# Kernel optimization log

Measured on AMD Instinct MI355X. Metric: run time of the kernel, lower is better.

The kernel has to match this reference:

```python
import jax, jax.numpy as jnp
import numpy as np

D = 256          # embed_dim
NH = 4           # num_heads
NE = 16          # num_hyperedges
TC = 512         # text_channels
WIN = 64         # window size
EPS = 1e-5


def setup_inputs() -> dict:
    key = jax.random.key(0)
    ks = jax.random.split(key, 20)
    s = 0.02
    return {
        "feature_map": jax.random.normal(ks[0], (8, 256, 64, 64), jnp.float32),
        "text_features": jax.random.normal(ks[1], (8, 64, TC), jnp.float32),
        # qkv_gen: Conv2d(256->256,1x1), GELU, Conv2d(256->768,3x3,pad1), GroupNorm(4,768)
        "conv1_w": jax.random.normal(ks[2], (D, 256, 1, 1), jnp.float32) * s,
        "conv1_b": jnp.zeros((D,), jnp.float32),
        "conv2_w": jax.random.normal(ks[3], (3 * D, D, 3, 3), jnp.float32) * s,
        "conv2_b": jnp.zeros((3 * D,), jnp.float32),
        "gn_w": jnp.ones((3 * D,), jnp.float32),
        "gn_b": jnp.zeros((3 * D,), jnp.float32),
        # shared nn.MultiheadAttention params
        "in_proj_w": jax.random.normal(ks[4], (3 * D, D), jnp.float32) * s,
        "in_proj_b": jnp.zeros((3 * D,), jnp.float32),
        "out_proj_w": jax.random.normal(ks[5], (D, D), jnp.float32) * s,
        "out_proj_b": jnp.zeros((D,), jnp.float32),
        # text_adapter Linear(512->256)
        "txt_w": jax.random.normal(ks[6], (D, TC), jnp.float32) * s,
        "txt_b": jnp.zeros((D,), jnp.float32),
        # edge_predictor: Linear(512->256), GELU, Linear(256->16)
        "ep1_w": jax.random.normal(ks[7], (D, 2 * D), jnp.float32) * s,
        "ep1_b": jnp.zeros((D,), jnp.float32),
        "ep2_w": jax.random.normal(ks[8], (NE, D), jnp.float32) * s,
        "ep2_b": jnp.zeros((NE,), jnp.float32),
    }


def _gelu(x):
    return jax.nn.gelu(x, approximate=False)  # torch default is exact erf GELU


def _conv(x, w, b, pad):
    y = jax.lax.conv_general_dilated(x, w, (1, 1), [(pad, pad), (pad, pad)],
                                     dimension_numbers=("NCHW", "OIHW", "NCHW"))
    return y + b[None, :, None, None]


def _group_norm(x, w, b, groups=4):
    B, C, H, W = x.shape
    xg = x.reshape(B, groups, C // groups, H, W)
    mu = xg.mean(axis=(2, 3, 4), keepdims=True)
    var = xg.var(axis=(2, 3, 4), keepdims=True)
    xg = (xg - mu) * jax.lax.rsqrt(var + EPS)
    return xg.reshape(B, C, H, W) * w[None, :, None, None] + b[None, :, None, None]


def _mha(q, k, v, in_w, in_b, out_w, out_b):
    # torch nn.MultiheadAttention (batch_first), same-dim q/k/v
    Wq, Wk, Wv = in_w[:D], in_w[D:2 * D], in_w[2 * D:]
    bq, bk, bv = in_b[:D], in_b[D:2 * D], in_b[2 * D:]
    dh = D // NH

    def split(x, W, bias):
        y = x @ W.T + bias                      # [B,L,D]
        Bv, L, _ = y.shape
        return y.reshape(Bv, L, NH, dh).transpose(0, 2, 1, 3)  # [B,H,L,dh]

    qh, kh, vh = split(q, Wq, bq), split(k, Wk, bk), split(v, Wv, bv)
    scores = jnp.einsum("bhqd,bhkd->bhqk", qh, kh) / jnp.sqrt(jnp.float32(dh))
    attn = jax.nn.softmax(scores, axis=-1)
    o = jnp.einsum("bhqk,bhkd->bhqd", attn, vh)
    Bv, _, Lq, _ = o.shape
    o = o.transpose(0, 2, 1, 3).reshape(Bv, Lq, D)
    return o @ out_w.T + out_b


def reference(feature_map, text_features, conv1_w, conv1_b, conv2_w, conv2_b,
              gn_w, gn_b, in_proj_w, in_proj_b, out_proj_w, out_proj_b,
              txt_w, txt_b, ep1_w, ep1_b, ep2_w, ep2_b):
    B, C, H, W = feature_map.shape
    N = H * W
    # qkv_gen
    x = _gelu(_conv(feature_map, conv1_w, conv1_b, 0))
    qkv = _group_norm(_conv(x, conv2_w, conv2_b, 1), gn_w, gn_b)
    q, k, v = jnp.split(qkv, 3, axis=1)                    # each [B,D,H,W]
    to_seq = lambda t: t.reshape(B, D, N).transpose(0, 2, 1)  # [B,N,D]
    q_seq, k_seq, v_seq = to_seq(q), to_seq(k), to_seq(v)

    # text_adapter: Linear then AdaptiveAvgPool1d(4) over sequence (L=64 -> 4 bins of 16)
    t = text_features @ txt_w.T + txt_b                    # [B,L,D]
    L = t.shape[1]
    text_feat = t.reshape(B, 4, L // 4, D).mean(axis=2)    # [B,4,D]

    # hierarchical attention
    nw = N // WIN
    q_win = q_seq.reshape(B * nw, WIN, D)
    k_win = k_seq.reshape(B * nw, WIN, D)
    v_win = v_seq.reshape(B * nw, WIN, D)
    local = _mha(q_win, k_win, v_win, in_proj_w, in_proj_b, out_proj_w, out_proj_b)
    local = local.reshape(B, nw, WIN, D)
    global_q = local.mean(axis=2)                          # [B,nw,D]
    glob = _mha(global_q, text_feat, text_feat, in_proj_w, in_proj_b, out_proj_w, out_proj_b)
    glob = jnp.broadcast_to(glob[:, :, None, :], (B, nw, WIN, D))

    combined = jnp.concatenate([local.reshape(B, N, D), glob.reshape(B, N, D)], axis=-1)
    h = _gelu(combined @ ep1_w.T + ep1_b)
    return jax.nn.sigmoid(h @ ep2_w.T + ep2_b)             # [B,N,16]
```

## Files before the change

### kernel.cpp

```cpp
#include <hip/hip_runtime.h>

#define DEV __device__ __forceinline__

typedef __attribute__((ext_vector_type(8))) short bfx8;
typedef __attribute__((ext_vector_type(4))) float fx4;

typedef __attribute__((address_space(3))) unsigned int as3_u32;
typedef const __attribute__((address_space(1))) unsigned int as1_u32c;

DEV void gl_lds16(const void* g, const void* l) {
  __builtin_amdgcn_global_load_lds((as1_u32c*)(unsigned long long)g,
                                   (as3_u32*)(unsigned long long)l, 16, 0, 0);
}

DEV short f2bf(float f) {
  unsigned u = __float_as_uint(f);
  u += 0x7fffu + ((u >> 16) & 1u);
  return (short)(u >> 16);
}
DEV float bf2f(short s) {
  return __uint_as_float(((unsigned)(unsigned short)s) << 16);
}
DEV float gelu_f(float x) { return 0.5f * x * (1.0f + erff(x * 0.70710678118654752f)); }

#define MFMA16(acc, a, b) (acc) = __builtin_amdgcn_mfma_f32_16x16x32_bf16((a), (b), (acc), 0, 0, 0)

struct CvtSeg { const float* src; short* dst; int n; };
struct CvtArgs { CvtSeg s[7]; };

__global__ __launch_bounds__(256) void cvt_multi(CvtArgs a) {
  CvtSeg s = a.s[blockIdx.y];
  int i = ((int)blockIdx.x * 256 + (int)threadIdx.x) * 8;
  if (i >= s.n) return;
  bfx8 o;
  #pragma unroll
  for (int j = 0; j < 8; ++j) o[j] = f2bf(s.src[i + j]);
  *(bfx8*)(s.dst + i) = o;
}

__global__ __launch_bounds__(256) void cvt_conv2w(const float* src, short* dst) {
  int oc = (int)blockIdx.x * 256 + (int)threadIdx.x;
  const float* s = src + (long)oc * 9;
  float t[9];
  #pragma unroll
  for (int j = 0; j < 9; ++j) t[j] = s[j];
  #pragma unroll
  for (int tap = 0; tap < 9; ++tap)
    dst[(long)tap * (768 * 256) + oc] = f2bf(t[tap]);
}

__global__ __launch_bounds__(64) void ebc2(const float* e1w, const float* e1b, const float* ob, float* ebc) {
  int n = blockIdx.x, lane = threadIdx.x;
  float s = 0.0f;
  #pragma unroll
  for (int i = 0; i < 4; ++i) {
    int c = lane + 64 * i;
    s += ob[c] * e1w[(long)n * 512 + c];
  }
  #pragma unroll
  for (int off = 1; off < 64; off <<= 1) s += __shfl_xor(s, off);
  if (lane == 0) ebc[n] = e1b[n] + s;
}

__global__ __launch_bounds__(256) void wcombk(const float* ow, const short* Wep1, short* Wcomb) {
  __shared__ short Bt[64 * 264];
  const int t = threadIdx.x;
  const int lane = t & 63, w = t >> 6;
  const int lg = lane >> 4, li = lane & 15;
  const int m0 = blockIdx.y * 64, n0 = blockIdx.x * 64;
  for (int idx = t; idx < 64 * 256; idx += 256) {
    int c = idx >> 6, d = idx & 63;
    Bt[d * 264 + c] = f2bf(ow[(long)c * 256 + n0 + d]);
  }
  __syncthreads();
  fx4 acc[4] = {};
  const short* aR = Wep1 + (long)(m0 + w * 16 + li) * 512 + lg * 8;
  for (int kc = 0; kc < 256; kc += 32) {
    bfx8 a = *(const bfx8*)(aR + kc);
    #pragma unroll
    for (int ni = 0; ni < 4; ++ni) {
      bfx8 bv = *(const bfx8*)(&Bt[(ni * 16 + li) * 264 + kc + lg * 8]);
      MFMA16(acc[ni], a, bv);
    }
  }
  #pragma unroll
  for (int ni = 0; ni < 4; ++ni)
    #pragma unroll
    for (int r = 0; r < 4; ++r)
      Wcomb[(long)(m0 + w * 16 + 4 * lg + r) * 256 + n0 + ni * 16 + li] = f2bf(acc[ni][r]);
}

DEV int axc(int p, int c) { return p * 260 + (c ^ (((p >> 2) & 7) << 2)); }

__global__ __launch_bounds__(256) void tc1(const float* fm, const short* W1bf,
                                           const float* b1, short* xP) {
  __shared__ float Af[64 * 260];
  const int lane = threadIdx.x & 63, wv = threadIdx.x >> 6;
  const int lg = lane >> 4, li = lane & 15;
  const int y = blockIdx.x & 63, b = blockIdx.x >> 6;
  const int t = threadIdx.x;
  short* dstP = xP + ((long)b * 66 * 66 + (long)(y + 1) * 66 + 1) * 256;
  const bfx8 z8 = {0, 0, 0, 0, 0, 0, 0, 0};

  if (t < 64) {
    if (t < 32) *(bfx8*)(dstP - 256 + t * 8) = z8;
    else        *(bfx8*)(dstP + 64 * 256 + (t - 32) * 8) = z8;
  }
  if (y == 0) {
    short* top = xP + (long)b * 66 * 66 * 256;
    for (int i = t; i < 2112; i += 256) *(bfx8*)(top + i * 8) = z8;
  }
  if (y == 63) {
    short* bot = xP + ((long)b * 66 * 66 + 65 * 66) * 256;
    for (int i = t; i < 2112; i += 256) *(bfx8*)(bot + i * 8) = z8;
  }

  const float* src = fm + (long)b * 256 * 4096 + y * 64;
  #pragma unroll
  for (int i = 0; i < 16; ++i) {
    int chunk = i * 256 + t;
    int c = chunk >> 4;
    int q = chunk & 15;
    fx4 v = *(const fx4*)(src + (long)c * 4096 + q * 4);
    #pragma unroll
    for (int j = 0; j < 4; ++j) Af[axc(q * 4 + j, c)] = v[j];
  }
  __syncthreads();

  fx4 acc[4][4] = {};
  const short* Bb = W1bf + (long)(wv * 64 + li) * 256 + lg * 8;
  for (int c0 = 0; c0 < 256; c0 += 32) {
    bfx8 af[4], bfr[4];
    #pragma unroll
    for (int mi = 0; mi < 4; ++mi) {
      int p = mi * 16 + li;
      fx4 lo = *(const fx4*)(&Af[axc(p, c0 + lg * 8)]);
      fx4 hi = *(const fx4*)(&Af[axc(p, c0 + lg * 8 + 4)]);
      bfx8 tt;
      tt[0] = f2bf(lo[0]); tt[1] = f2bf(lo[1]); tt[2] = f2bf(lo[2]); tt[3] = f2bf(lo[3]);
      tt[4] = f2bf(hi[0]); tt[5] = f2bf(hi[1]); tt[6] = f2bf(hi[2]); tt[7] = f2bf(hi[3]);
      af[mi] = tt;
    }
    #pragma unroll
    for (int ni = 0; ni < 4; ++ni) bfr[ni] = *(const bfx8*)(Bb + ni * 16 * 256 + c0);
    #pragma unroll
    for (int mi = 0; mi < 4; ++mi)
      #pragma unroll
      for (int ni = 0; ni < 4; ++ni) MFMA16(acc[mi][ni], af[mi], bfr[ni]);
  }

  #pragma unroll
  for (int mi = 0; mi < 4; ++mi)
    #pragma unroll
    for (int ni = 0; ni < 4; ++ni) {
      int col = wv * 64 + ni * 16 + li;
      float bias = b1[col];
      #pragma unroll
      for (int r = 0; r < 4; ++r) {
        int x = mi * 16 + 4 * lg + r;
        dstP[(long)x * 256 + col] = f2bf(gelu_f(acc[mi][ni][r] + bias));
      }
    }
}

struct GemmP {
  const short* A; const short* B; void* O;
  const float* biasN; const float* biasM; const float* rowbias;
  long lda, ldb, ldo, sA, sB, sO;
  int M, N, K, outF32, act, padHW;
  int aShift;
  long sBN, sBM;
};

DEV void gemm_body(const GemmP& g, int bx, int by, int bz) {
  __shared__ short As[128 * 32];
  __shared__ short Bs[128 * 32];
  const int lane = threadIdx.x & 63, wv = threadIdx.x >> 6;
  const int wm = wv >> 1, wn = wv & 1;
  const int lg = lane >> 4, li = lane & 15;
  const int m0 = by * 128, n0 = bx * 128, z = bz;
  const short* A = g.A + (long)z * g.sA + (long)(n0 >> 8) * g.aShift;
  const short* B = g.B + (long)z * g.sB;
  const int srow = wv * 16 + (lane >> 2);
  const int scol = (lane & 3) * 8;
  const short* pA0 = A + (long)(m0 + srow) * g.lda + scol;
  const short* pA1 = A + (long)(m0 + 64 + srow) * g.lda + scol;
  const short* pB0 = B + (long)(n0 + srow) * g.ldb + scol;
  const short* pB1 = B + (long)(n0 + 64 + srow) * g.ldb + scol;
  short* ldsA = As + wv * 512;
  short* ldsB = Bs + wv * 512;
  const short* aRd = As + (wm * 64 + li) * 32 + lg * 8;
  const short* bRd = Bs + (wn * 64 + li) * 32 + lg * 8;

  fx4 acc[4][4] = {};
  for (int kc = 0; kc < g.K; kc += 32) {
    gl_lds16(pA0 + kc, ldsA);
    gl_lds16(pA1 + kc, ldsA + 2048);
    gl_lds16(pB0 + kc, ldsB);
    gl_lds16(pB1 + kc, ldsB + 2048);
    __syncthreads();
    bfx8 af[4], bf[4];
    #pragma unroll
    for (int mi = 0; mi < 4; ++mi) af[mi] = *(const bfx8*)(aRd + mi * 16 * 32);
    #pragma unroll
    for (int ni = 0; ni < 4; ++ni) bf[ni] = *(const bfx8*)(bRd + ni * 16 * 32);
    #pragma unroll
    for (int mi = 0; mi < 4; ++mi)
      #pragma unroll
      for (int ni = 0; ni < 4; ++ni)
        MFMA16(acc[mi][ni], af[mi], bf[ni]);
    __syncthreads();
  }

  #pragma unroll
  for (int mi = 0; mi < 4; ++mi)
    #pragma unroll
    for (int ni = 0; ni < 4; ++ni) {
      int col = n0 + wn * 64 + ni * 16 + li;
      int rowb = m0 + wm * 64 + mi * 16 + 4 * lg;
      float bn = g.biasN ? g.biasN[(long)z * g.sBN + col] : 0.0f;
      #pragma unroll
      for (int r = 0; r < 4; ++r) {
        int row = rowb + r;
        float v = acc[mi][ni][r] + bn;
        if (g.biasM) v += g.biasM[(long)z * g.sBM + row];
        if (g.act == 1) v = gelu_f(v);
        long oidx = (long)z * g.sO + (long)row * g.ldo + col;
        if (g.outF32) ((float*)g.O)[oidx] = v;
        else ((short*)g.O)[oidx] = f2bf(v);
      }
    }
}

__global__ __launch_bounds__(256) void projk(GemmP gq, GemmP gv) {
  int bid = (int)blockIdx.x;
  int id = (bid & 7) * 192 + (bid >> 3);
  if (id < 1024) {
    int z = id >> 7, r = id & 127;
    gemm_body(gq, r & 3, r >> 2, z);
  } else {
    int j = id - 1024;
    int z = j >> 6, r = j & 63;
    gemm_body(gv, r & 31, r >> 5, z);
  }
}

__global__ __launch_bounds__(256) void conv2g(const short* xP, const short* W2t,
                                              const float* b2, short* qkv, float* stats) {
  __shared__ short As[2 * 128 * 32];
  __shared__ short Bs[2 * 128 * 32];
  __shared__ float red[4][4];
  const int lane = threadIdx.x & 63, wv = threadIdx.x >> 6;
  const int wm = wv >> 1, wn = wv & 1;
  const int lg = lane >> 4, li = lane & 15;
  const int w = ((int)blockIdx.x & 7) * 192 + ((int)blockIdx.x >> 3);
  const int n0 = (w % 6) * 128;
  const int by = w / 6;
  const int b = by >> 5, ypair = by & 31;
  const short* xPb = xP + (long)b * 66 * 66 * 256;

  const int srow = wv * 16 + (lane >> 2);
  const int scol = (lane & 3) * 8;
  long baseA[2], baseB[2];
  #pragma unroll
  for (int j = 0; j < 2; ++j) {
    int r = j * 64 + srow;
    int yy = 2 * ypair + (r >> 6);
    int x = r & 63;
    baseA[j] = ((long)yy * 66 + x) * 256 + scol;
    baseB[j] = (long)(n0 + r) * 256 + scol;
  }
  short* ldsA = As + wv * 512;
  short* ldsB = Bs + wv * 512;
  const short* aRd = As + (wm * 64 + li) * 32 + lg * 8;
  const short* bRd = Bs + (wn * 64 + li) * 32 + lg * 8;

  fx4 acc[4][4] = {};
  for (int ks = 0; ks < 36; ++ks) {
    int tap = ks >> 2;
    int c0 = (ks & 3) * 64;
    int dy = tap / 3, dx = tap - dy * 3;
    long aoff = (long)(dy * 66 + dx) * 256 + c0;
    long boff = (long)tap * (768 * 256) + c0;
    gl_lds16(xPb + baseA[0] + aoff, ldsA);
    gl_lds16(xPb + baseA[1] + aoff, ldsA + 2048);
    gl_lds16(xPb + baseA[0] + aoff + 32, ldsA + 4096);
    gl_lds16(xPb + baseA[1] + aoff + 32, ldsA + 6144);
    gl_lds16(W2t + baseB[0] + boff, ldsB);
    gl_lds16(W2t + baseB[1] + boff, ldsB + 2048);
    gl_lds16(W2t + baseB[0] + boff + 32, ldsB + 4096);
    gl_lds16(W2t + baseB[1] + boff + 32, ldsB + 6144);
    __syncthreads();
    #pragma unroll
    for (int kk = 0; kk < 2; ++kk) {
      bfx8 af[4], bf[4];
      #pragma unroll
      for (int mi = 0; mi < 4; ++mi) af[mi] = *(const bfx8*)(aRd + kk * 4096 + mi * 16 * 32);
      #pragma unroll
      for (int ni = 0; ni < 4; ++ni) bf[ni] = *(const bfx8*)(bRd + kk * 4096 + ni * 16 * 32);
      #pragma unroll
      for (int mi = 0; mi < 4; ++mi)
        #pragma unroll
        for (int ni = 0; ni < 4; ++ni)
          MFMA16(acc[mi][ni], af[mi], bf[ni]);
    }
    __syncthreads();
  }

  const int g0 = n0 / 192;
  const int bnd = (g0 + 1) * 192;
  float sA = 0.0f, s2A = 0.0f, sB = 0.0f, s2B = 0.0f;
  const long prow0 = (long)b * 4096 + (long)ypair * 128 + wm * 64 + 4 * lg;
  #pragma unroll
  for (int ni = 0; ni < 4; ++ni) {
    int col = n0 + wn * 64 + ni * 16 + li;
    float bias = b2[col];
    bool inA = (col < bnd);
    #pragma unroll
    for (int mi = 0; mi < 4; ++mi) {
      long rb = prow0 + mi * 16;
      #pragma unroll
      for (int r = 0; r < 4; ++r) {
        float v = acc[mi][ni][r] + bias;
        if (inA) { sA += v; s2A += v * v; } else { sB += v; s2B += v * v; }
        qkv[(rb + r) * 768 + col] = f2bf(v);
      }
    }
  }
  #pragma unroll
  for (int off = 1; off < 64; off <<= 1) {
    sA += __shfl_xor(sA, off);  s2A += __shfl_xor(s2A, off);
    sB += __shfl_xor(sB, off);  s2B += __shfl_xor(s2B, off);
  }
  if (lane == 0) { red[wv][0] = sA; red[wv][1] = s2A; red[wv][2] = sB; red[wv][3] = s2B; }
  __syncthreads();
  if (threadIdx.x == 0) {
    float a1 = red[0][0] + red[1][0] + red[2][0] + red[3][0];
    float a2 = red[0][1] + red[1][1] + red[2][1] + red[3][1];
    atomicAdd(&stats[(b * 4 + g0) * 2], a1);
    atomicAdd(&stats[(b * 4 + g0) * 2 + 1], a2);
    if (bnd < n0 + 128) {
      float b1s = red[0][2] + red[1][2] + red[2][2] + red[3][2];
      float b2s = red[0][3] + red[1][3] + red[2][3] + red[3][3];
      atomicAdd(&stats[(b * 4 + g0 + 1) * 2], b1s);
      atomicAdd(&stats[(b * 4 + g0 + 1) * 2 + 1], b2s);
    }
  }
}

__global__ __launch_bounds__(256) void gn_fold(const float* stats, const float* gnw, const float* gnb,
                                               const float* inw, const float* inb,
                                               short* Wf, float* bfold) {
  const int lane = threadIdx.x & 63, wv = threadIdx.x >> 6;
  const int row = blockIdx.x * 4 + wv;
  const int b = row / 768, j = row - b * 768;
  const int cb = (j >> 8) << 8;
  const float nrm = 1.0f / (192.0f * 4096.0f);
  float part = 0.0f;
  #pragma unroll
  for (int i = 0; i < 4; ++i) {
    int c = lane + 64 * i;
    int cg = cb + c;
    int grp = cg / 192;
    float s1 = stats[(b * 4 + grp) * 2];
    float s2 = stats[(b * 4 + grp) * 2 + 1];
    float mu = s1 * nrm;
    float var = s2 * nrm - mu * mu;
    float rs = rsqrtf(var + 1e-5f);
    float s = rs * gnw[cg];
    float t = gnb[cg] - mu * s;
    float wv_ = inw[(long)j * 256 + c];
    Wf[(long)row * 256 + c] = f2bf(wv_ * s);
    part += t * wv_;
  }
  #pragma unroll
  for (int off = 1; off < 64; off <<= 1) part += __shfl_xor(part, off);
  if (lane == 0) bfold[row] = inb[j] + part;
}

__global__ __launch_bounds__(256) void globk_txt(const short* Tbf, const short* Wtxt,
                                                 const short* Wqkv, const float* tb,
                                                 const float* inb, float* khv, float* vhv) {
  __shared__ float tmean_s[4][512];
  __shared__ float tfb_s[4][256];
  const int t = threadIdx.x;
  const int b = blockIdx.x;
  {
    int key = t >> 6, d0 = (t & 63) * 8;
    float s[8] = {};
    const short* src = Tbf + ((long)(b * 64 + key * 16)) * 512 + d0;
    for (int i = 0; i < 16; ++i) {
      bfx8 v = *(const bfx8*)(src + i * 512);
      #pragma unroll
      for (int j = 0; j < 8; ++j) s[j] += bf2f(v[j]);
    }
    #pragma unroll
    for (int j = 0; j < 8; ++j) tmean_s[key][d0 + j] = s[j] * (1.0f / 16.0f);
  }
  __syncthreads();
  {
    int n = t;
    float a0 = 0, a1 = 0, a2 = 0, a3 = 0;
    const short* wr = Wtxt + (long)n * 512;
    for (int d = 0; d < 512; d += 8) {
      bfx8 w = *(const bfx8*)(wr + d);
      #pragma unroll
      for (int j = 0; j < 8; ++j) {
        float wf = bf2f(w[j]);
        a0 += tmean_s[0][d + j] * wf;
        a1 += tmean_s[1][d + j] * wf;
        a2 += tmean_s[2][d + j] * wf;
        a3 += tmean_s[3][d + j] * wf;
      }
    }
    float bias = tb[n];
    tfb_s[0][n] = a0 + bias; tfb_s[1][n] = a1 + bias;
    tfb_s[2][n] = a2 + bias; tfb_s[3][n] = a3 + bias;
  }
  __syncthreads();
  {
    int n = t;
    const short* wk = Wqkv + (long)(256 + n) * 256;
    const short* wvp = Wqkv + (long)(512 + n) * 256;
    float k0=0,k1=0,k2=0,k3=0,v0=0,v1=0,v2=0,v3=0;
    for (int d = 0; d < 256; d += 8) {
      bfx8 wkv = *(const bfx8*)(wk + d);
      bfx8 wvv = *(const bfx8*)(wvp + d);
      #pragma unroll
      for (int j = 0; j < 8; ++j) {
        float f0 = tfb_s[0][d+j], f1 = tfb_s[1][d+j], f2 = tfb_s[2][d+j], f3 = tfb_s[3][d+j];
        float kw = bf2f(wkv[j]), vw = bf2f(wvv[j]);
        k0 += f0*kw; k1 += f1*kw; k2 += f2*kw; k3 += f3*kw;
        v0 += f0*vw; v1 += f1*vw; v2 += f2*vw; v3 += f3*vw;
      }
    }
    float bk = inb[256+n], bv = inb[512+n];
    khv[(b*4+0)*256+n]=k0+bk; khv[(b*4+1)*256+n]=k1+bk;
    khv[(b*4+2)*256+n]=k2+bk; khv[(b*4+3)*256+n]=k3+bk;
    vhv[(b*4+0)*256+n]=v0+bv; vhv[(b*4+1)*256+n]=v1+bv;
    vhv[(b*4+2)*256+n]=v2+bv; vhv[(b*4+3)*256+n]=v3+bv;
  }
}

__global__ __launch_bounds__(256) void attn_local(const short* qk, const short* vhT,
                                                  short* oat, short* oatm) {
  __shared__ short Pl[4 * 64 * 72];
  const int lane = threadIdx.x & 63, h = threadIdx.x >> 6;
  const int lg = lane >> 4, li = lane & 15;
  const int bw = blockIdx.x;
  const int b = bw >> 6, wY = bw & 63;
  const long p0 = (long)bw * 64;

  bfx8 qf[4][2], kf[4][2];
  #pragma unroll
  for (int mi = 0; mi < 4; ++mi)
    #pragma unroll
    for (int ks = 0; ks < 2; ++ks) {
      qf[mi][ks] = *(const bfx8*)(qk + (p0 + 16 * mi + li) * 512 + h * 64 + 32 * ks + 8 * lg);
      kf[mi][ks] = *(const bfx8*)(qk + (p0 + 16 * mi + li) * 512 + 256 + h * 64 + 32 * ks + 8 * lg);
    }
  fx4 s[4][4] = {};
  #pragma unroll
  for (int mi = 0; mi < 4; ++mi)
    #pragma unroll
    for (int ni = 0; ni < 4; ++ni) {
      MFMA16(s[mi][ni], qf[mi][0], kf[ni][0]);
      MFMA16(s[mi][ni], qf[mi][1], kf[ni][1]);
    }
  #pragma unroll
  for (int mi = 0; mi < 4; ++mi)
    #pragma unroll
    for (int ni = 0; ni < 4; ++ni) s[mi][ni] *= 0.125f;

  #pragma unroll
  for (int mi = 0; mi < 4; ++mi)
    #pragma unroll
    for (int r = 0; r < 4; ++r) {
      float mx = fmaxf(fmaxf(s[mi][0][r], s[mi][1][r]), fmaxf(s[mi][2][r], s[mi][3][r]));
      for (int off = 1; off < 16; off <<= 1) mx = fmaxf(mx, __shfl_xor(mx, off));
      float e[4];
      float sum = 0.0f;
      #pragma unroll
      for (int ni = 0; ni < 4; ++ni) { e[ni] = expf(s[mi][ni][r] - mx); sum += e[ni]; }
      for (int off = 1; off < 16; off <<= 1) sum += __shfl_xor(sum, off);
      float inv = 1.0f / sum;
      int row = h * 64 + 16 * mi + 4 * lg + r;
      #pragma unroll
      for (int ni = 0; ni < 4; ++ni) Pl[row * 72 + 16 * ni + li] = f2bf(e[ni] * inv);
    }
  __syncthreads();

  fx4 o[4][4] = {};
  #pragma unroll
  for (int ks = 0; ks < 2; ++ks) {
    bfx8 pf[4], vf[4];
    #pragma unroll
    for (int mi = 0; mi < 4; ++mi)
      pf[mi] = *(const bfx8*)(&Pl[(h * 64 + 16 * mi + li) * 72 + 32 * ks + 8 * lg]);
    #pragma unroll
    for (int ni = 0; ni < 4; ++ni)
      vf[ni] = *(const bfx8*)(vhT + ((long)(b * 256 + h * 64 + 16 * ni + li)) * 4096 + wY * 64 + 32 * ks + 8 * lg);
    #pragma unroll
    for (int mi = 0; mi < 4; ++mi)
      #pragma unroll
      for (int ni = 0; ni < 4; ++ni) MFMA16(o[mi][ni], pf[mi], vf[ni]);
  }
  #pragma unroll
  for (int mi = 0; mi < 4; ++mi)
    #pragma unroll
    for (int ni = 0; ni < 4; ++ni)
      #pragma unroll
      for (int r = 0; r < 4; ++r)
        oat[(p0 + 16 * mi + 4 * lg + r) * 256 + h * 64 + 16 * ni + li] = f2bf(o[mi][ni][r]);

  #pragma unroll
  for (int ni = 0; ni < 4; ++ni) {
    float s2 = 0.0f;
    #pragma unroll
    for (int mi = 0; mi < 4; ++mi)
      #pragma unroll
      for (int r = 0; r < 4; ++r) s2 += o[mi][ni][r];
    s2 += __shfl_xor(s2, 16);
    s2 += __shfl_xor(s2, 32);
    if (lg == 0)
      oatm[(long)bw * 256 + h * 64 + 16 * ni + li] = f2bf(s2 * (1.0f / 64.0f));
  }
}

#define GP 272

DEV void mm_stage(const short* srcA, const short* Bw, long ldb, const float* biasN,
                  short* dstL, float* dstG, int wv, int lg, int li) {
  fx4 acc[4][4] = {};
  const short* aRd = srcA + li * GP + lg * 8;
  const short* bR = Bw + (long)(wv * 64 + li) * ldb + lg * 8;
  for (int kc = 0; kc < 256; kc += 32) {
    bfx8 af[4], bf[4];
    #pragma unroll
    for (int mi = 0; mi < 4; ++mi) af[mi] = *(const bfx8*)(aRd + mi * 16 * GP + kc);
    #pragma unroll
    for (int ni = 0; ni < 4; ++ni) bf[ni] = *(const bfx8*)(bR + (long)ni * 16 * ldb + kc);
    #pragma unroll
    for (int mi = 0; mi < 4; ++mi)
      #pragma unroll
      for (int ni = 0; ni < 4; ++ni) MFMA16(acc[mi][ni], af[mi], bf[ni]);
  }
  #pragma unroll
  for (int mi = 0; mi < 4; ++mi)
    #pragma unroll
    for (int ni = 0; ni < 4; ++ni) {
      int col = wv * 64 + ni * 16 + li;
      float bn = biasN[col];
      #pragma unroll
      for (int r = 0; r < 4; ++r) {
        int row = mi * 16 + 4 * lg + r;
        float v = acc[mi][ni][r] + bn;
        if (dstL) dstL[row * GP + col] = f2bf(v);
        else dstG[(long)row * 256 + col] = v;
      }
    }
}

__global__ __launch_bounds__(256) void globk2(
    const short* oatm, const float* khv, const float* vhv,
    const short* Wo, const short* Wqkv, const short* Wep1,
    const float* ob, const float* inb, const float* ebc,
    float* gcon) {
  __shared__ short bufA[64 * GP];
  __shared__ short bufB[64 * GP];
  __shared__ float kh_s[4][256];
  __shared__ float vh_s[4][256];
  __shared__ float scb[16], pb[16];
  const int t = threadIdx.x;
  const int lane = t & 63, wv = t >> 6;
  const int lg = lane >> 4, li = lane & 15;
  const int b = blockIdx.x;

  {
    #pragma unroll
    for (int i = 0; i < 8; ++i) {
      int chunk = i * 256 + t;
      int row = chunk >> 5, colc = (chunk & 31) * 8;
      *(bfx8*)(bufA + row * GP + colc) =
          *(const bfx8*)(oatm + ((long)(b * 64 + row)) * 256 + colc);
    }
    #pragma unroll
    for (int key = 0; key < 4; ++key) {
      kh_s[key][t] = khv[(long)(b * 4 + key) * 256 + t];
      vh_s[key][t] = vhv[(long)(b * 4 + key) * 256 + t];
    }
  }
  __syncthreads();
  mm_stage(bufA, Wo, 256, ob, bufB, nullptr, wv, lg, li);
  __syncthreads();
  mm_stage(bufB, Wqkv, 256, inb, bufA, nullptr, wv, lg, li);
  __syncthreads();
  {
    int p = t >> 2, h = t & 3;
    const short* qr = bufA + p * GP + h * 64;
    float sc[4];
    #pragma unroll
    for (int key = 0; key < 4; ++key) {
      float s = 0.0f;
      for (int d = 0; d < 64; d += 8) {
        bfx8 q8 = *(const bfx8*)(qr + d);
        #pragma unroll
        for (int j = 0; j < 8; ++j) s += bf2f(q8[j]) * kh_s[key][h * 64 + d + j];
      }
      sc[key] = s * 0.125f;
    }
    float mx = fmaxf(fmaxf(sc[0], sc[1]), fmaxf(sc[2], sc[3]));
    float e0 = expf(sc[0]-mx), e1 = expf(sc[1]-mx), e2 = expf(sc[2]-mx), e3 = expf(sc[3]-mx);
    float inv = 1.0f / (e0 + e1 + e2 + e3);
    e0 *= inv; e1 *= inv; e2 *= inv; e3 *= inv;
    short* orow = bufB + p * GP + h * 64;
    for (int d = 0; d < 64; ++d) {
      float o = e0*vh_s[0][h*64+d] + e1*vh_s[1][h*64+d] + e2*vh_s[2][h*64+d] + e3*vh_s[3][h*64+d];
      orow[d] = f2bf(o);
    }
  }
  __syncthreads();
  mm_stage(bufB, Wo, 256, ob, bufA, nullptr, wv, lg, li);
  __syncthreads();
  mm_stage(bufA, Wep1 + 256, 512, ebc, nullptr, gcon + (long)b * 64 * 256, wv, lg, li);
}

__global__ __launch_bounds__(256) void ep12(const short* oat, const short* Wcomb,
                                            const short* Wep2, const float* gcon,
                                            const float* e2b, float* out) {
  __shared__ short As[128 * 32];
  __shared__ short Bs[128 * 32];
  __shared__ short hl[128 * 140];
  const int lane = threadIdx.x & 63, wv = threadIdx.x >> 6;
  const int wm = wv >> 1, wn = wv & 1;
  const int lg = lane >> 4, li = lane & 15;
  const int m0 = (int)blockIdx.x * 128;
  const int srow = wv * 16 + (lane >> 2);
  const int scol = (lane & 3) * 8;
  const short* pA0 = oat + (long)(m0 + srow) * 256 + scol;
  const short* pA1 = oat + (long)(m0 + 64 + srow) * 256 + scol;
  short* ldsA = As + wv * 512;
  short* ldsB = Bs + wv * 512;
  const short* aRd = As + (wm * 64 + li) * 32 + lg * 8;
  const short* bRd = Bs + (wn * 64 + li) * 32 + lg * 8;

  fx4 eacc[2] = {};
  for (int half = 0; half < 2; ++half) {
    const short* B = Wcomb + (long)(half * 128) * 256;
    const short* pB0 = B + (long)srow * 256 + scol;
    const short* pB1 = B + (long)(64 + srow) * 256 + scol;
    fx4 acc[4][4] = {};
    for (int kc = 0; kc < 256; kc += 32) {
      gl_lds16(pA0 + kc, ldsA);
      gl_lds16(pA1 + kc, ldsA + 2048);
      gl_lds16(pB0 + kc, ldsB);
      gl_lds16(pB1 + kc, ldsB + 2048);
      __syncthreads();
      bfx8 af[4], bf[4];
      #pragma unroll
      for (int mi = 0; mi < 4; ++mi) af[mi] = *(const bfx8*)(aRd + mi * 16 * 32);
      #pragma unroll
      for (int ni = 0; ni < 4; ++ni) bf[ni] = *(const bfx8*)(bRd + ni * 16 * 32);
      #pragma unroll
      for (int mi = 0; mi < 4; ++mi)
        #pragma unroll
        for (int ni = 0; ni < 4; ++ni)
          MFMA16(acc[mi][ni], af[mi], bf[ni]);
      __syncthreads();
    }
    #pragma unroll
    for (int mi = 0; mi < 4; ++mi)
      #pragma unroll
      for (int ni = 0; ni < 4; ++ni) {
        int coll = wn * 64 + ni * 16 + li;
        int colg = half * 128 + coll;
        #pragma unroll
        for (int r = 0; r < 4; ++r) {
          int rowl = wm * 64 + mi * 16 + 4 * lg + r;
          float v = acc[mi][ni][r] + gcon[(long)((m0 + rowl) >> 6) * 256 + colg];
          hl[rowl * 140 + coll] = f2bf(gelu_f(v));
        }
      }
    __syncthreads();
    #pragma unroll
    for (int kc = 0; kc < 128; kc += 32) {
      bfx8 bf2v = *(const bfx8*)(Wep2 + (long)li * 256 + half * 128 + kc + lg * 8);
      #pragma unroll
      for (int mi = 0; mi < 2; ++mi) {
        bfx8 af = *(const bfx8*)(hl + (wv * 32 + mi * 16 + li) * 140 + kc + lg * 8);
        MFMA16(eacc[mi], af, bf2v);
      }
    }
    __syncthreads();
  }
  #pragma unroll
  for (int mi = 0; mi < 2; ++mi)
    #pragma unroll
    for (int r = 0; r < 4; ++r) {
      int row = m0 + wv * 32 + mi * 16 + 4 * lg + r;
      out[(long)row * 16 + li] = 1.0f / (1.0f + expf(-(eacc[mi][r] + e2b[li])));
    }
}

extern "C" void kernel_launch(void* const* d_in, const int* in_sizes, int n_in,
                              void* d_out, int out_size, void* d_ws, size_t ws_size,
                              hipStream_t stream) {
  (void)in_sizes; (void)n_in; (void)out_size; (void)ws_size;
  const float* fm  = (const float*)d_in[0];
  const float* txt = (const float*)d_in[1];
  const float* w1  = (const float*)d_in[2];
  const float* b1  = (const float*)d_in[3];
  const float* w2  = (const float*)d_in[4];
  const float* b2  = (const float*)d_in[5];
  const float* gnw = (const float*)d_in[6];
  const float* gnb = (const float*)d_in[7];
  const float* inw = (const float*)d_in[8];
  const float* inb = (const float*)d_in[9];
  const float* ow  = (const float*)d_in[10];
  const float* ob  = (const float*)d_in[11];
  const float* tw  = (const float*)d_in[12];
  const float* tb  = (const float*)d_in[13];
  const float* e1w = (const float*)d_in[14];
  const float* e1b = (const float*)d_in[15];
  const float* e2w = (const float*)d_in[16];
  const float* e2b = (const float*)d_in[17];
  float* out = (float*)d_out;

  char* base = (char*)d_ws;
  size_t off = 0;
  auto alloc = [&](size_t bytes) -> char* {
    char* r = base + off;
    off = (off + bytes + 255) & ~(size_t)255;
    return r;
  };
  short* W1bf = (short*)alloc(256 * 256 * 2);
  short* W2t  = (short*)alloc((size_t)9 * 768 * 256 * 2);
  short* Wqkv = (short*)alloc(768 * 256 * 2);
  short* Wo   = (short*)alloc(256 * 256 * 2);
  short* Wcomb= (short*)alloc(256 * 256 * 2);
  float* ebc  = (float*)alloc(256 * 4);
  short* Wtxt = (short*)alloc(256 * 512 * 2);
  short* Wep1 = (short*)alloc(256 * 512 * 2);
  short* Wep2 = (short*)alloc(16 * 256 * 2);
  short* Tbf  = (short*)alloc((size_t)8 * 64 * 512 * 2);
  short* xP   = (short*)alloc((size_t)8 * 66 * 66 * 256 * 2);
  short* qkv  = (short*)alloc((size_t)8 * 4096 * 768 * 2);
  float* stats= (float*)alloc(64 * 4);
  short* Wf   = (short*)alloc((size_t)8 * 768 * 256 * 2);
  float* bfold= (float*)alloc((size_t)8 * 768 * 4);
  short* qk   = (short*)alloc((size_t)32768 * 512 * 2);
  short* vhT  = (short*)alloc((size_t)8 * 4096 * 256 * 2);
  short* oat  = (short*)alloc((size_t)8 * 4096 * 256 * 2);
  short* oatm = (short*)alloc(512 * 256 * 2);
  float* khv  = (float*)alloc(8 * 4 * 256 * 4);
  float* vhv  = (float*)alloc(8 * 4 * 256 * 4);
  float* gcon = (float*)alloc(512 * 256 * 4);

  hipMemsetAsync(stats, 0, 64 * 4, stream);

  CvtArgs ca;
  ca.s[0] = {w1,  W1bf, 256 * 256};
  ca.s[1] = {inw, Wqkv, 768 * 256};
  ca.s[2] = {ow,  Wo,   256 * 256};
  ca.s[3] = {tw,  Wtxt, 256 * 512};
  ca.s[4] = {e1w, Wep1, 256 * 512};
  ca.s[5] = {e2w, Wep2, 16 * 256};
  ca.s[6] = {txt, Tbf,  8 * 64 * 512};
  cvt_multi<<<dim3(128, 7), 256, 0, stream>>>(ca);
  cvt_conv2w<<<768, 256, 0, stream>>>(w2, W2t);
  ebc2<<<256, 64, 0, stream>>>(e1w, e1b, ob, ebc);
  globk_txt<<<8, 256, 0, stream>>>(Tbf, Wtxt, Wqkv, tb, inb, khv, vhv);
  wcombk<<<dim3(4, 4), 256, 0, stream>>>(ow, Wep1, Wcomb);

  tc1<<<512, 256, 0, stream>>>(fm, W1bf, b1, xP);

  conv2g<<<1536, 256, 0, stream>>>(xP, W2t, b2, qkv, stats);

  gn_fold<<<1536, 256, 0, stream>>>(stats, gnw, gnb, inw, inb, Wf, bfold);

  {
    GemmP gq{};
    gq.A = qkv; gq.lda = 768; gq.sA = 4096L * 768;
    gq.B = Wf; gq.ldb = 256; gq.sB = 768L * 256;
    gq.O = qk; gq.ldo = 512; gq.sO = 4096L * 512;
    gq.biasN = bfold; gq.sBN = 768;
    gq.aShift = 256;
    gq.M = 4096; gq.N = 512; gq.K = 256;
    GemmP gv{};
    gv.A = Wf + 512 * 256; gv.lda = 256; gv.sA = 768L * 256;
    gv.B = qkv + 512; gv.ldb = 768; gv.sB = 4096L * 768;
    gv.O = vhT; gv.ldo = 4096; gv.sO = 256L * 4096;
    gv.biasM = bfold + 512; gv.sBM = 768;
    gv.M = 256; gv.N = 4096; gv.K = 256;
    projk<<<1536, 256, 0, stream>>>(gq, gv);
  }

  attn_local<<<512, 256, 0, stream>>>(qk, vhT, oat, oatm);

  globk2<<<8, 256, 0, stream>>>(oatm, khv, vhv, Wo, Wqkv, Wep1, ob, inb, ebc, gcon);

  ep12<<<256, 256, 0, stream>>>(oat, Wcomb, Wep2, gcon, e2b, out);
}
```

Before: 328.5 us.

## Merge prep kernels, fuse global attention into local attention, deepen GEMM K-step

Folds the five weight-conversion and text-projection kernels into one multi-role prep kernel, with the text path computed from fp32 inputs directly so the text-to-bf16 conversion is gone. The global-attention kernel now runs as the tail of the local-attention kernel: the last block per batch, picked by an atomic counter, does the global stage. GEMM and ep12 main loops load 64-wide K slices per barrier instead of 32, and the conv2 loop uses incremental offsets instead of per-iteration division. The aim is fewer launches, fewer barriers and fewer serialized tiny kernels, at the cost of larger LDS use and a counter-based handoff that relies on threadfences.

```diff
diff --git a/kernel.cpp b/kernel.cpp
--- a/kernel.cpp
+++ b/kernel.cpp
@@ -25,69 +25,142 @@
 
 #define MFMA16(acc, a, b) (acc) = __builtin_amdgcn_mfma_f32_16x16x32_bf16((a), (b), (acc), 0, 0, 0)
 
-struct CvtSeg { const float* src; short* dst; int n; };
-struct CvtArgs { CvtSeg s[7]; };
-
-__global__ __launch_bounds__(256) void cvt_multi(CvtArgs a) {
-  CvtSeg s = a.s[blockIdx.y];
-  int i = ((int)blockIdx.x * 256 + (int)threadIdx.x) * 8;
-  if (i >= s.n) return;
-  bfx8 o;
-  #pragma unroll
-  for (int j = 0; j < 8; ++j) o[j] = f2bf(s.src[i + j]);
-  *(bfx8*)(s.dst + i) = o;
-}
-
-__global__ __launch_bounds__(256) void cvt_conv2w(const float* src, short* dst) {
-  int oc = (int)blockIdx.x * 256 + (int)threadIdx.x;
-  const float* s = src + (long)oc * 9;
-  float t[9];
-  #pragma unroll
-  for (int j = 0; j < 9; ++j) t[j] = s[j];
-  #pragma unroll
-  for (int tap = 0; tap < 9; ++tap)
-    dst[(long)tap * (768 * 256) + oc] = f2bf(t[tap]);
-}
-
-__global__ __launch_bounds__(64) void ebc2(const float* e1w, const float* e1b, const float* ob, float* ebc) {
-  int n = blockIdx.x, lane = threadIdx.x;
-  float s = 0.0f;
-  #pragma unroll
-  for (int i = 0; i < 4; ++i) {
-    int c = lane + 64 * i;
-    s += ob[c] * e1w[(long)n * 512 + c];
-  }
-  #pragma unroll
-  for (int off = 1; off < 64; off <<= 1) s += __shfl_xor(s, off);
-  if (lane == 0) ebc[n] = e1b[n] + s;
-}
-
-__global__ __launch_bounds__(256) void wcombk(const float* ow, const short* Wep1, short* Wcomb) {
-  __shared__ short Bt[64 * 264];
+struct PrepArgs {
+  const float *w1, *inw, *ow, *tw, *e1w, *e2w, *txt, *w2, *e1b, *ob, *tb, *inb;
+  short *W1bf, *Wqkv, *Wo, *Wtxt, *Wep1, *Wep2, *W2t, *Wcomb;
+  float *ebc, *khv, *vhv;
+};
+
+__global__ __launch_bounds__(256) void prep(PrepArgs a) {
+  __shared__ char shmem[34816];
+  const int bid = (int)blockIdx.x;
   const int t = threadIdx.x;
-  const int lane = t & 63, w = t >> 6;
-  const int lg = lane >> 4, li = lane & 15;
-  const int m0 = blockIdx.y * 64, n0 = blockIdx.x * 64;
-  for (int idx = t; idx < 64 * 256; idx += 256) {
-    int c = idx >> 6, d = idx & 63;
-    Bt[d * 264 + c] = f2bf(ow[(long)c * 256 + n0 + d]);
-  }
-  __syncthreads();
-  fx4 acc[4] = {};
-  const short* aR = Wep1 + (long)(m0 + w * 16 + li) * 512 + lg * 8;
-  for (int kc = 0; kc < 256; kc += 32) {
-    bfx8 a = *(const bfx8*)(aR + kc);
-    #pragma unroll
-    for (int ni = 0; ni < 4; ++ni) {
-      bfx8 bv = *(const bfx8*)(&Bt[(ni * 16 + li) * 264 + kc + lg * 8]);
-      MFMA16(acc[ni], a, bv);
-    }
-  }
-  #pragma unroll
-  for (int ni = 0; ni < 4; ++ni)
-    #pragma unroll
-    for (int r = 0; r < 4; ++r)
-      Wcomb[(long)(m0 + w * 16 + 4 * lg + r) * 256 + n0 + ni * 16 + li] = f2bf(acc[ni][r]);
+  if (bid < 290) {
+    const float* src; short* dst; int st;
+    if (bid < 32)       { src = a.w1;  dst = a.W1bf; st = 0; }
+    else if (bid < 128) { src = a.inw; dst = a.Wqkv; st = 32; }
+    else if (bid < 160) { src = a.ow;  dst = a.Wo;   st = 128; }
+    else if (bid < 224) { src = a.tw;  dst = a.Wtxt; st = 160; }
+    else if (bid < 288) { src = a.e1w; dst = a.Wep1; st = 224; }
+    else                { src = a.e2w; dst = a.Wep2; st = 288; }
+    long i = ((long)(bid - st) * 256 + t) * 8;
+    bfx8 o;
+    #pragma unroll
+    for (int j = 0; j < 8; ++j) o[j] = f2bf(src[i + j]);
+    *(bfx8*)(dst + i) = o;
+  } else if (bid < 1058) {
+    int oc = (bid - 290) * 256 + t;
+    const float* s = a.w2 + (long)oc * 9;
+    float v[9];
+    #pragma unroll
+    for (int j = 0; j < 9; ++j) v[j] = s[j];
+    #pragma unroll
+    for (int tap = 0; tap < 9; ++tap)
+      a.W2t[(long)tap * (768 * 256) + oc] = f2bf(v[tap]);
+  } else if (bid < 1122) {
+    int n = (bid - 1058) * 4 + (t >> 6);
+    int lane = t & 63;
+    float s = 0.0f;
+    #pragma unroll
+    for (int i = 0; i < 4; ++i) {
+      int c = lane + 64 * i;
+      s += a.ob[c] * a.e1w[(long)n * 512 + c];
+    }
+    #pragma unroll
+    for (int off = 1; off < 64; off <<= 1) s += __shfl_xor(s, off);
+    if (lane == 0) a.ebc[n] = a.e1b[n] + s;
+  } else if (bid < 1130) {
+    float* tmean = (float*)shmem;
+    float* tfb = (float*)(shmem + 8192);
+    const int b = bid - 1122;
+    {
+      int key = t >> 6, d0 = (t & 63) * 8;
+      float s[8] = {};
+      const float* src = a.txt + ((long)(b * 64 + key * 16)) * 512 + d0;
+      for (int i = 0; i < 16; ++i) {
+        fx4 v0 = *(const fx4*)(src + (long)i * 512);
+        fx4 v1 = *(const fx4*)(src + (long)i * 512 + 4);
+        #pragma unroll
+        for (int j = 0; j < 4; ++j) { s[j] += v0[j]; s[4 + j] += v1[j]; }
+      }
+      #pragma unroll
+      for (int j = 0; j < 8; ++j) tmean[key * 512 + d0 + j] = s[j] * (1.0f / 16.0f);
+    }
+    __syncthreads();
+    {
+      int n = t;
+      float a0 = 0, a1 = 0, a2 = 0, a3 = 0;
+      const float* wr = a.tw + (long)n * 512;
+      for (int d = 0; d < 512; d += 4) {
+        fx4 w = *(const fx4*)(wr + d);
+        #pragma unroll
+        for (int j = 0; j < 4; ++j) {
+          float wf = w[j];
+          a0 += tmean[0 * 512 + d + j] * wf;
+          a1 += tmean[1 * 512 + d + j] * wf;
+          a2 += tmean[2 * 512 + d + j] * wf;
+          a3 += tmean[3 * 512 + d + j] * wf;
+        }
+      }
+      float bias = a.tb[n];
+      tfb[0 * 256 + n] = a0 + bias; tfb[1 * 256 + n] = a1 + bias;
+      tfb[2 * 256 + n] = a2 + bias; tfb[3 * 256 + n] = a3 + bias;
+    }
+    __syncthreads();
+    {
+      int n = t;
+      const float* wk = a.inw + (long)(256 + n) * 256;
+      const float* wvp = a.inw + (long)(512 + n) * 256;
+      float k0=0,k1=0,k2=0,k3=0,v0=0,v1=0,v2=0,v3=0;
+      for (int d = 0; d < 256; d += 4) {
+        fx4 wkv = *(const fx4*)(wk + d);
+        fx4 wvv = *(const fx4*)(wvp + d);
+        #pragma unroll
+        for (int j = 0; j < 4; ++j) {
+          float f0 = tfb[0*256+d+j], f1 = tfb[1*256+d+j], f2 = tfb[2*256+d+j], f3 = tfb[3*256+d+j];
+          float kw = wkv[j], vw = wvv[j];
+          k0 += f0*kw; k1 += f1*kw; k2 += f2*kw; k3 += f3*kw;
+          v0 += f0*vw; v1 += f1*vw; v2 += f2*vw; v3 += f3*vw;
+        }
+      }
+      float bk = a.inb[256+n], bv = a.inb[512+n];
+      a.khv[(b*4+0)*256+n]=k0+bk; a.khv[(b*4+1)*256+n]=k1+bk;
+      a.khv[(b*4+2)*256+n]=k2+bk; a.khv[(b*4+3)*256+n]=k3+bk;
+      a.vhv[(b*4+0)*256+n]=v0+bv; a.vhv[(b*4+1)*256+n]=v1+bv;
+      a.vhv[(b*4+2)*256+n]=v2+bv; a.vhv[(b*4+3)*256+n]=v3+bv;
+    }
+  } else {
+    short* Bt = (short*)shmem;
+    const int idx = bid - 1130;
+    const int bx = idx & 3, by = idx >> 2;
+    const int lane = t & 63, w = t >> 6;
+    const int lg = lane >> 4, li = lane & 15;
+    const int m0 = by * 64, n0 = bx * 64;
+    for (int id2 = t; id2 < 64 * 256; id2 += 256) {
+      int c = id2 >> 6, d = id2 & 63;
+      Bt[d * 264 + c] = f2bf(a.ow[(long)c * 256 + n0 + d]);
+    }
+    __syncthreads();
+    fx4 acc[4] = {};
+    const float* aR = a.e1w + (long)(m0 + w * 16 + li) * 512 + lg * 8;
+    for (int kc = 0; kc < 256; kc += 32) {
+      fx4 lo = *(const fx4*)(aR + kc);
+      fx4 hi = *(const fx4*)(aR + kc + 4);
+      bfx8 av;
+      av[0] = f2bf(lo[0]); av[1] = f2bf(lo[1]); av[2] = f2bf(lo[2]); av[3] = f2bf(lo[3]);
+      av[4] = f2bf(hi[0]); av[5] = f2bf(hi[1]); av[6] = f2bf(hi[2]); av[7] = f2bf(hi[3]);
+      #pragma unroll
+      for (int ni = 0; ni < 4; ++ni) {
+        bfx8 bv = *(const bfx8*)(&Bt[(ni * 16 + li) * 264 + kc + lg * 8]);
+        MFMA16(acc[ni], av, bv);
+      }
+    }
+    #pragma unroll
+    for (int ni = 0; ni < 4; ++ni)
+      #pragma unroll
+      for (int r = 0; r < 4; ++r)
+        a.Wcomb[(long)(m0 + w * 16 + 4 * lg + r) * 256 + n0 + ni * 16 + li] = f2bf(acc[ni][r]);
+  }
 }
 
 DEV int axc(int p, int c) { return p * 260 + (c ^ (((p >> 2) & 7) << 2)); }
@@ -165,16 +238,16 @@
 
 struct GemmP {
   const short* A; const short* B; void* O;
-  const float* biasN; const float* biasM; const float* rowbias;
+  const float* biasN; const float* biasM;
   long lda, ldb, ldo, sA, sB, sO;
-  int M, N, K, outF32, act, padHW;
+  int M, N, K, outF32, act;
   int aShift;
   long sBN, sBM;
 };
 
-DEV void gemm_body(const GemmP& g, int bx, int by, int bz) {
-  __shared__ short As[128 * 32];
-  __shared__ short Bs[128 * 32];
+DEV void gemm_body64(const GemmP& g, int bx, int by, int bz) {
+  __shared__ short As[2 * 128 * 32];
+  __shared__ short Bs[2 * 128 * 32];
   const int lane = threadIdx.x & 63, wv = threadIdx.x >> 6;
   const int wm = wv >> 1, wn = wv & 1;
   const int lg = lane >> 4, li = lane & 15;
@@ -193,22 +266,29 @@
   const short* bRd = Bs + (wn * 64 + li) * 32 + lg * 8;
 
   fx4 acc[4][4] = {};
-  for (int kc = 0; kc < g.K; kc += 32) {
+  for (int kc = 0; kc < g.K; kc += 64) {
     gl_lds16(pA0 + kc, ldsA);
     gl_lds16(pA1 + kc, ldsA + 2048);
+    gl_lds16(pA0 + kc + 32, ldsA + 4096);
+    gl_lds16(pA1 + kc + 32, ldsA + 6144);
     gl_lds16(pB0 + kc, ldsB);
     gl_lds16(pB1 + kc, ldsB + 2048);
+    gl_lds16(pB0 + kc + 32, ldsB + 4096);
+    gl_lds16(pB1 + kc + 32, ldsB + 6144);
     __syncthreads();
-    bfx8 af[4], bf[4];
-    #pragma unroll
-    for (int mi = 0; mi < 4; ++mi) af[mi] = *(const bfx8*)(aRd + mi * 16 * 32);
-    #pragma unroll
-    for (int ni = 0; ni < 4; ++ni) bf[ni] = *(const bfx8*)(bRd + ni * 16 * 32);
-    #pragma unroll
-    for (int mi = 0; mi < 4; ++mi)
-      #pragma unroll
-      for (int ni = 0; ni < 4; ++ni)
-        MFMA16(acc[mi][ni], af[mi], bf[ni]);
+    #pragma unroll
+    for (int kk = 0; kk < 2; ++kk) {
+      bfx8 af[4], bf[4];
+      #pragma unroll
+      for (int mi = 0; mi < 4; ++mi) af[mi] = *(const bfx8*)(aRd + kk * 4096 + mi * 16 * 32);
+      #pragma unroll
+      for (int ni = 0; ni < 4; ++ni) bf[ni] = *(const bfx8*)(bRd + kk * 4096 + ni * 16 * 32);
+      #pragma unroll
+      for (int mi = 0; mi < 4; ++mi)
+        #pragma unroll
+        for (int ni = 0; ni < 4; ++ni)
+          MFMA16(acc[mi][ni], af[mi], bf[ni]);
+    }
     __syncthreads();
   }
 
@@ -237,11 +317,11 @@
   int id = (bid & 7) * 192 + (bid >> 3);
   if (id < 1024) {
     int z = id >> 7, r = id & 127;
-    gemm_body(gq, r & 3, r >> 2, z);
+    gemm_body64(gq, r & 3, r >> 2, z);
   } else {
     int j = id - 1024;
     int z = j >> 6, r = j & 63;
-    gemm_body(gv, r & 31, r >> 5, z);
+    gemm_body64(gv, r & 31, r >> 5, z);
   }
 }
 
@@ -276,12 +356,9 @@
   const short* bRd = Bs + (wn * 64 + li) * 32 + lg * 8;
 
   fx4 acc[4][4] = {};
+  long aoff = 0, boff = 0;
+  int txc = 0;
   for (int ks = 0; ks < 36; ++ks) {
-    int tap = ks >> 2;
-    int c0 = (ks & 3) * 64;
-    int dy = tap / 3, dx = tap - dy * 3;
-    long aoff = (long)(dy * 66 + dx) * 256 + c0;
-    long boff = (long)tap * (768 * 256) + c0;
     gl_lds16(xPb + baseA[0] + aoff, ldsA);
     gl_lds16(xPb + baseA[1] + aoff, ldsA + 2048);
     gl_lds16(xPb + baseA[0] + aoff + 32, ldsA + 4096);
@@ -305,6 +382,12 @@
           MFMA16(acc[mi][ni], af[mi], bf[ni]);
     }
     __syncthreads();
+    aoff += 64; boff += 64;
+    if ((ks & 3) == 3) {
+      boff += 196608 - 256;
+      if (txc == 2) { aoff += 16128; txc = 0; }
+      else ++txc;
+    }
   }
 
   const int g0 = n0 / 192;
@@ -378,155 +461,6 @@
   if (lane == 0) bfold[row] = inb[j] + part;
 }
 
-__global__ __launch_bounds__(256) void globk_txt(const short* Tbf, const short* Wtxt,
-                                                 const short* Wqkv, const float* tb,
-                                                 const float* inb, float* khv, float* vhv) {
-  __shared__ float tmean_s[4][512];
-  __shared__ float tfb_s[4][256];
-  const int t = threadIdx.x;
-  const int b = blockIdx.x;
-  {
-    int key = t >> 6, d0 = (t & 63) * 8;
-    float s[8] = {};
-    const short* src = Tbf + ((long)(b * 64 + key * 16)) * 512 + d0;
-    for (int i = 0; i < 16; ++i) {
-      bfx8 v = *(const bfx8*)(src + i * 512);
-      #pragma unroll
-      for (int j = 0; j < 8; ++j) s[j] += bf2f(v[j]);
-    }
-    #pragma unroll
-    for (int j = 0; j < 8; ++j) tmean_s[key][d0 + j] = s[j] * (1.0f / 16.0f);
-  }
-  __syncthreads();
-  {
-    int n = t;
-    float a0 = 0, a1 = 0, a2 = 0, a3 = 0;
-    const short* wr = Wtxt + (long)n * 512;
-    for (int d = 0; d < 512; d += 8) {
-      bfx8 w = *(const bfx8*)(wr + d);
-      #pragma unroll
-      for (int j = 0; j < 8; ++j) {
-        float wf = bf2f(w[j]);
-        a0 += tmean_s[0][d + j] * wf;
-        a1 += tmean_s[1][d + j] * wf;
-        a2 += tmean_s[2][d + j] * wf;
-        a3 += tmean_s[3][d + j] * wf;
-      }
-    }
-    float bias = tb[n];
-    tfb_s[0][n] = a0 + bias; tfb_s[1][n] = a1 + bias;
-    tfb_s[2][n] = a2 + bias; tfb_s[3][n] = a3 + bias;
-  }
-  __syncthreads();
-  {
-    int n = t;
-    const short* wk = Wqkv + (long)(256 + n) * 256;
-    const short* wvp = Wqkv + (long)(512 + n) * 256;
-    float k0=0,k1=0,k2=0,k3=0,v0=0,v1=0,v2=0,v3=0;
-    for (int d = 0; d < 256; d += 8) {
-      bfx8 wkv = *(const bfx8*)(wk + d);
-      bfx8 wvv = *(const bfx8*)(wvp + d);
-      #pragma unroll
-      for (int j = 0; j < 8; ++j) {
-        float f0 = tfb_s[0][d+j], f1 = tfb_s[1][d+j], f2 = tfb_s[2][d+j], f3 = tfb_s[3][d+j];
-        float kw = bf2f(wkv[j]), vw = bf2f(wvv[j]);
-        k0 += f0*kw; k1 += f1*kw; k2 += f2*kw; k3 += f3*kw;
-        v0 += f0*vw; v1 += f1*vw; v2 += f2*vw; v3 += f3*vw;
-      }
-    }
-    float bk = inb[256+n], bv = inb[512+n];
-    khv[(b*4+0)*256+n]=k0+bk; khv[(b*4+1)*256+n]=k1+bk;
-    khv[(b*4+2)*256+n]=k2+bk; khv[(b*4+3)*256+n]=k3+bk;
-    vhv[(b*4+0)*256+n]=v0+bv; vhv[(b*4+1)*256+n]=v1+bv;
-    vhv[(b*4+2)*256+n]=v2+bv; vhv[(b*4+3)*256+n]=v3+bv;
-  }
-}
-
-__global__ __launch_bounds__(256) void attn_local(const short* qk, const short* vhT,
-                                                  short* oat, short* oatm) {
-  __shared__ short Pl[4 * 64 * 72];
-  const int lane = threadIdx.x & 63, h = threadIdx.x >> 6;
-  const int lg = lane >> 4, li = lane & 15;
-  const int bw = blockIdx.x;
-  const int b = bw >> 6, wY = bw & 63;
-  const long p0 = (long)bw * 64;
-
-  bfx8 qf[4][2], kf[4][2];
-  #pragma unroll
-  for (int mi = 0; mi < 4; ++mi)
-    #pragma unroll
-    for (int ks = 0; ks < 2; ++ks) {
-      qf[mi][ks] = *(const bfx8*)(qk + (p0 + 16 * mi + li) * 512 + h * 64 + 32 * ks + 8 * lg);
-      kf[mi][ks] = *(const bfx8*)(qk + (p0 + 16 * mi + li) * 512 + 256 + h * 64 + 32 * ks + 8 * lg);
-    }
-  fx4 s[4][4] = {};
-  #pragma unroll
-  for (int mi = 0; mi < 4; ++mi)
-    #pragma unroll
-    for (int ni = 0; ni < 4; ++ni) {
-      MFMA16(s[mi][ni], qf[mi][0], kf[ni][0]);
-      MFMA16(s[mi][ni], qf[mi][1], kf[ni][1]);
-    }
-  #pragma unroll
-  for (int mi = 0; mi < 4; ++mi)
-    #pragma unroll
-    for (int ni = 0; ni < 4; ++ni) s[mi][ni] *= 0.125f;
-
-  #pragma unroll
-  for (int mi = 0; mi < 4; ++mi)
-    #pragma unroll
-    for (int r = 0; r < 4; ++r) {
-      float mx = fmaxf(fmaxf(s[mi][0][r], s[mi][1][r]), fmaxf(s[mi][2][r], s[mi][3][r]));
-      for (int off = 1; off < 16; off <<= 1) mx = fmaxf(mx, __shfl_xor(mx, off));
-      float e[4];
-      float sum = 0.0f;
-      #pragma unroll
-      for (int ni = 0; ni < 4; ++ni) { e[ni] = expf(s[mi][ni][r] - mx); sum += e[ni]; }
-      for (int off = 1; off < 16; off <<= 1) sum += __shfl_xor(sum, off);
-      float inv = 1.0f / sum;
-      int row = h * 64 + 16 * mi + 4 * lg + r;
-      #pragma unroll
-      for (int ni = 0; ni < 4; ++ni) Pl[row * 72 + 16 * ni + li] = f2bf(e[ni] * inv);
-    }
-  __syncthreads();
-
-  fx4 o[4][4] = {};
-  #pragma unroll
-  for (int ks = 0; ks < 2; ++ks) {
-    bfx8 pf[4], vf[4];
-    #pragma unroll
-    for (int mi = 0; mi < 4; ++mi)
-      pf[mi] = *(const bfx8*)(&Pl[(h * 64 + 16 * mi + li) * 72 + 32 * ks + 8 * lg]);
-    #pragma unroll
-    for (int ni = 0; ni < 4; ++ni)
-      vf[ni] = *(const bfx8*)(vhT + ((long)(b * 256 + h * 64 + 16 * ni + li)) * 4096 + wY * 64 + 32 * ks + 8 * lg);
-    #pragma unroll
-    for (int mi = 0; mi < 4; ++mi)
-      #pragma unroll
-      for (int ni = 0; ni < 4; ++ni) MFMA16(o[mi][ni], pf[mi], vf[ni]);
-  }
-  #pragma unroll
-  for (int mi = 0; mi < 4; ++mi)
-    #pragma unroll
-    for (int ni = 0; ni < 4; ++ni)
-      #pragma unroll
-      for (int r = 0; r < 4; ++r)
-        oat[(p0 + 16 * mi + 4 * lg + r) * 256 + h * 64 + 16 * ni + li] = f2bf(o[mi][ni][r]);
-
-  #pragma unroll
-  for (int ni = 0; ni < 4; ++ni) {
-    float s2 = 0.0f;
-    #pragma unroll
-    for (int mi = 0; mi < 4; ++mi)
-      #pragma unroll
-      for (int r = 0; r < 4; ++r) s2 += o[mi][ni][r];
-    s2 += __shfl_xor(s2, 16);
-    s2 += __shfl_xor(s2, 32);
-    if (lg == 0)
-      oatm[(long)bw * 256 + h * 64 + 16 * ni + li] = f2bf(s2 * (1.0f / 64.0f));
-  }
-}
-
 #define GP 272
 
 DEV void mm_stage(const short* srcA, const short* Bw, long ldb, const float* biasN,
@@ -561,75 +495,170 @@
     }
 }
 
-__global__ __launch_bounds__(256) void globk2(
-    const short* oatm, const float* khv, const float* vhv,
+union ShU {
+  short Pl[4 * 64 * 72];
+  struct {
+    short bufA[64 * GP];
+    short bufB[64 * GP];
+    float kh[4][256];
+    float vh[4][256];
+    float scb[16];
+    float pb[16];
+  } g;
+};
+
+__global__ __launch_bounds__(256) void attn_lg(
+    const short* qk, const short* vhT, const float* khv, const float* vhv,
     const short* Wo, const short* Wqkv, const short* Wep1,
     const float* ob, const float* inb, const float* ebc,
-    float* gcon) {
-  __shared__ short bufA[64 * GP];
-  __shared__ short bufB[64 * GP];
-  __shared__ float kh_s[4][256];
-  __shared__ float vh_s[4][256];
-  __shared__ float scb[16], pb[16];
+    short* oat, short* oatm, float* gcon, int* cnt) {
+  __shared__ ShU sh;
+  __shared__ int elect_s;
   const int t = threadIdx.x;
-  const int lane = t & 63, wv = t >> 6;
+  const int lane = t & 63, h = t >> 6;
   const int lg = lane >> 4, li = lane & 15;
-  const int b = blockIdx.x;
-
+  const int bw = blockIdx.x;
+  const int b = bw >> 6, wY = bw & 63;
+  const long p0 = (long)bw * 64;
+
+  bfx8 qf[4][2], kf[4][2];
+  #pragma unroll
+  for (int mi = 0; mi < 4; ++mi)
+    #pragma unroll
+    for (int ks = 0; ks < 2; ++ks) {
+      qf[mi][ks] = *(const bfx8*)(qk + (p0 + 16 * mi + li) * 512 + h * 64 + 32 * ks + 8 * lg);
+      kf[mi][ks] = *(const bfx8*)(qk + (p0 + 16 * mi + li) * 512 + 256 + h * 64 + 32 * ks + 8 * lg);
+    }
+  fx4 s[4][4] = {};
+  #pragma unroll
+  for (int mi = 0; mi < 4; ++mi)
+    #pragma unroll
+    for (int ni = 0; ni < 4; ++ni) {
+      MFMA16(s[mi][ni], qf[mi][0], kf[ni][0]);
+      MFMA16(s[mi][ni], qf[mi][1], kf[ni][1]);
+    }
+  #pragma unroll
+  for (int mi = 0; mi < 4; ++mi)
+    #pragma unroll
+    for (int ni = 0; ni < 4; ++ni) s[mi][ni] *= 0.125f;
+
+  #pragma unroll
+  for (int mi = 0; mi < 4; ++mi)
+    #pragma unroll
+    for (int r = 0; r < 4; ++r) {
+      float mx = fmaxf(fmaxf(s[mi][0][r], s[mi][1][r]), fmaxf(s[mi][2][r], s[mi][3][r]));
+      for (int off = 1; off < 16; off <<= 1) mx = fmaxf(mx, __shfl_xor(mx, off));
+      float e[4];
+      float sum = 0.0f;
+      #pragma unroll
+      for (int ni = 0; ni < 4; ++ni) { e[ni] = expf(s[mi][ni][r] - mx); sum += e[ni]; }
+      for (int off = 1; off < 16; off <<= 1) sum += __shfl_xor(sum, off);
+      float inv = 1.0f / sum;
+      int row = h * 64 + 16 * mi + 4 * lg + r;
+      #pragma unroll
+      for (int ni = 0; ni < 4; ++ni) sh.Pl[row * 72 + 16 * ni + li] = f2bf(e[ni] * inv);
+    }
+  __syncthreads();
+
+  fx4 o[4][4] = {};
+  #pragma unroll
+  for (int ks = 0; ks < 2; ++ks) {
+    bfx8 pf[4], vf[4];
+    #pragma unroll
+    for (int mi = 0; mi < 4; ++mi)
+      pf[mi] = *(const bfx8*)(&sh.Pl[(h * 64 + 16 * mi + li) * 72 + 32 * ks + 8 * lg]);
+    #pragma unroll
+    for (int ni = 0; ni < 4; ++ni)
+      vf[ni] = *(const bfx8*)(vhT + ((long)(b * 256 + h * 64 + 16 * ni + li)) * 4096 + wY * 64 + 32 * ks + 8 * lg);
+    #pragma unroll
+    for (int mi = 0; mi < 4; ++mi)
+      #pragma unroll
+      for (int ni = 0; ni < 4; ++ni) MFMA16(o[mi][ni], pf[mi], vf[ni]);
+  }
+  #pragma unroll
+  for (int mi = 0; mi < 4; ++mi)
+    #pragma unroll
+    for (int ni = 0; ni < 4; ++ni)
+      #pragma unroll
+      for (int r = 0; r < 4; ++r)
+        oat[(p0 + 16 * mi + 4 * lg + r) * 256 + h * 64 + 16 * ni + li] = f2bf(o[mi][ni][r]);
+
+  #pragma unroll
+  for (int ni = 0; ni < 4; ++ni) {
+    float s2 = 0.0f;
+    #pragma unroll
+    for (int mi = 0; mi < 4; ++mi)
+      #pragma unroll
+      for (int r = 0; r < 4; ++r) s2 += o[mi][ni][r];
+    s2 += __shfl_xor(s2, 16);
+    s2 += __shfl_xor(s2, 32);
+    if (lg == 0)
+      oatm[(long)bw * 256 + h * 64 + 16 * ni + li] = f2bf(s2 * (1.0f / 64.0f));
+  }
+
+  __threadfence();
+  __syncthreads();
+  if (t == 0) elect_s = (atomicAdd(&cnt[b], 1) == 63) ? 1 : 0;
+  __syncthreads();
+  if (!elect_s) return;
+  __threadfence();
+
+  const int wv = h;
   {
     #pragma unroll
     for (int i = 0; i < 8; ++i) {
       int chunk = i * 256 + t;
       int row = chunk >> 5, colc = (chunk & 31) * 8;
-      *(bfx8*)(bufA + row * GP + colc) =
+      *(bfx8*)(sh.g.bufA + row * GP + colc) =
           *(const bfx8*)(oatm + ((long)(b * 64 + row)) * 256 + colc);
     }
     #pragma unroll
     for (int key = 0; key < 4; ++key) {
-      kh_s[key][t] = khv[(long)(b * 4 + key) * 256 + t];
-      vh_s[key][t] = vhv[(long)(b * 4 + key) * 256 + t];
-    }
-  }
-  __syncthreads();
-  mm_stage(bufA, Wo, 256, ob, bufB, nullptr, wv, lg, li);
-  __syncthreads();
-  mm_stage(bufB, Wqkv, 256, inb, bufA, nullptr, wv, lg, li);
+      sh.g.kh[key][t] = khv[(long)(b * 4 + key) * 256 + t];
+      sh.g.vh[key][t] = vhv[(long)(b * 4 + key) * 256 + t];
+    }
+  }
+  __syncthreads();
+  mm_stage(sh.g.bufA, Wo, 256, ob, sh.g.bufB, nullptr, wv, lg, li);
+  __syncthreads();
+  mm_stage(sh.g.bufB, Wqkv, 256, inb, sh.g.bufA, nullptr, wv, lg, li);
   __syncthreads();
   {
-    int p = t >> 2, h = t & 3;
-    const short* qr = bufA + p * GP + h * 64;
+    int p = t >> 2, hh = t & 3;
+    const short* qr = sh.g.bufA + p * GP + hh * 64;
     float sc[4];
     #pragma unroll
     for (int key = 0; key < 4; ++key) {
-      float s = 0.0f;
+      float sum = 0.0f;
       for (int d = 0; d < 64; d += 8) {
         bfx8 q8 = *(const bfx8*)(qr + d);
         #pragma unroll
-        for (int j = 0; j < 8; ++j) s += bf2f(q8[j]) * kh_s[key][h * 64 + d + j];
-      }
-      sc[key] = s * 0.125f;
+        for (int j = 0; j < 8; ++j) sum += bf2f(q8[j]) * sh.g.kh[key][hh * 64 + d + j];
+      }
+      sc[key] = sum * 0.125f;
     }
     float mx = fmaxf(fmaxf(sc[0], sc[1]), fmaxf(sc[2], sc[3]));
     float e0 = expf(sc[0]-mx), e1 = expf(sc[1]-mx), e2 = expf(sc[2]-mx), e3 = expf(sc[3]-mx);
     float inv = 1.0f / (e0 + e1 + e2 + e3);
     e0 *= inv; e1 *= inv; e2 *= inv; e3 *= inv;
-    short* orow = bufB + p * GP + h * 64;
+    short* orow = sh.g.bufB + p * GP + hh * 64;
     for (int d = 0; d < 64; ++d) {
-      float o = e0*vh_s[0][h*64+d] + e1*vh_s[1][h*64+d] + e2*vh_s[2][h*64+d] + e3*vh_s[3][h*64+d];
-      orow[d] = f2bf(o);
-    }
-  }
-  __syncthreads();
-  mm_stage(bufB, Wo, 256, ob, bufA, nullptr, wv, lg, li);
-  __syncthreads();
-  mm_stage(bufA, Wep1 + 256, 512, ebc, nullptr, gcon + (long)b * 64 * 256, wv, lg, li);
+      float ov = e0*sh.g.vh[0][hh*64+d] + e1*sh.g.vh[1][hh*64+d] +
+                 e2*sh.g.vh[2][hh*64+d] + e3*sh.g.vh[3][hh*64+d];
+      orow[d] = f2bf(ov);
+    }
+  }
+  __syncthreads();
+  mm_stage(sh.g.bufB, Wo, 256, ob, sh.g.bufA, nullptr, wv, lg, li);
+  __syncthreads();
+  mm_stage(sh.g.bufA, Wep1 + 256, 512, ebc, nullptr, gcon + (long)b * 64 * 256, wv, lg, li);
 }
 
 __global__ __launch_bounds__(256) void ep12(const short* oat, const short* Wcomb,
                                             const short* Wep2, const float* gcon,
                                             const float* e2b, float* out) {
-  __shared__ short As[128 * 32];
-  __shared__ short Bs[128 * 32];
+  __shared__ short As[2 * 128 * 32];
+  __shared__ short Bs[2 * 128 * 32];
   __shared__ short hl[128 * 140];
   const int lane = threadIdx.x & 63, wv = threadIdx.x >> 6;
   const int wm = wv >> 1, wn = wv & 1;
@@ -650,22 +679,29 @@
     const short* pB0 = B + (long)srow * 256 + scol;
     const short* pB1 = B + (long)(64 + srow) * 256 + scol;
     fx4 acc[4][4] = {};
-    for (int kc = 0; kc < 256; kc += 32) {
+    for (int kc = 0; kc < 256; kc += 64) {
       gl_lds16(pA0 + kc, ldsA);
       gl_lds16(pA1 + kc, ldsA + 2048);
+      gl_lds16(pA0 + kc + 32, ldsA + 4096);
+      gl_lds16(pA1 + kc + 32, ldsA + 6144);
       gl_lds16(pB0 + kc, ldsB);
       gl_lds16(pB1 + kc, ldsB + 2048);
+      gl_lds16(pB0 + kc + 32, ldsB + 4096);
+      gl_lds16(pB1 + kc + 32, ldsB + 6144);
       __syncthreads();
-      bfx8 af[4], bf[4];
-      #pragma unroll
-      for (int mi = 0; mi < 4; ++mi) af[mi] = *(const bfx8*)(aRd + mi * 16 * 32);
-      #pragma unroll
-      for (int ni = 0; ni < 4; ++ni) bf[ni] = *(const bfx8*)(bRd + ni * 16 * 32);
-      #pragma unroll
-      for (int mi = 0; mi < 4; ++mi)
-        #pragma unroll
-        for (int ni = 0; ni < 4; ++ni)
-          MFMA16(acc[mi][ni], af[mi], bf[ni]);
+      #pragma unroll
+      for (int kk = 0; kk < 2; ++kk) {
+        bfx8 af[4], bf[4];
+        #pragma unroll
+        for (int mi = 0; mi < 4; ++mi) af[mi] = *(const bfx8*)(aRd + kk * 4096 + mi * 16 * 32);
+        #pragma unroll
+        for (int ni = 0; ni < 4; ++ni) bf[ni] = *(const bfx8*)(bRd + kk * 4096 + ni * 16 * 32);
+        #pragma unroll
+        for (int mi = 0; mi < 4; ++mi)
+          #pragma unroll
+          for (int ni = 0; ni < 4; ++ni)
+            MFMA16(acc[mi][ni], af[mi], bf[ni]);
+      }
       __syncthreads();
     }
     #pragma unroll
@@ -742,10 +778,11 @@
   short* Wtxt = (short*)alloc(256 * 512 * 2);
   short* Wep1 = (short*)alloc(256 * 512 * 2);
   short* Wep2 = (short*)alloc(16 * 256 * 2);
-  short* Tbf  = (short*)alloc((size_t)8 * 64 * 512 * 2);
   short* xP   = (short*)alloc((size_t)8 * 66 * 66 * 256 * 2);
   short* qkv  = (short*)alloc((size_t)8 * 4096 * 768 * 2);
-  float* stats= (float*)alloc(64 * 4);
+  float* zeros= (float*)alloc(96 * 4);
+  float* stats= zeros;
+  int*   cnt  = (int*)(zeros + 64);
   short* Wf   = (short*)alloc((size_t)8 * 768 * 256 * 2);
   float* bfold= (float*)alloc((size_t)8 * 768 * 4);
   short* qk   = (short*)alloc((size_t)32768 * 512 * 2);
@@ -756,21 +793,15 @@
   float* vhv  = (float*)alloc(8 * 4 * 256 * 4);
   float* gcon = (float*)alloc(512 * 256 * 4);
 
-  hipMemsetAsync(stats, 0, 64 * 4, stream);
-
-  CvtArgs ca;
-  ca.s[0] = {w1,  W1bf, 256 * 256};
-  ca.s[1] = {inw, Wqkv, 768 * 256};
-  ca.s[2] = {ow,  Wo,   256 * 256};
-  ca.s[3] = {tw,  Wtxt, 256 * 512};
-  ca.s[4] = {e1w, Wep1, 256 * 512};
-  ca.s[5] = {e2w, Wep2, 16 * 256};
-  ca.s[6] = {txt, Tbf,  8 * 64 * 512};
-  cvt_multi<<<dim3(128, 7), 256, 0, stream>>>(ca);
-  cvt_conv2w<<<768, 256, 0, stream>>>(w2, W2t);
-  ebc2<<<256, 64, 0, stream>>>(e1w, e1b, ob, ebc);
-  globk_txt<<<8, 256, 0, stream>>>(Tbf, Wtxt, Wqkv, tb, inb, khv, vhv);
-  wcombk<<<dim3(4, 4), 256, 0, stream>>>(ow, Wep1, Wcomb);
+  hipMemsetAsync(zeros, 0, 96 * 4, stream);
+
+  PrepArgs pa;
+  pa.w1 = w1; pa.inw = inw; pa.ow = ow; pa.tw = tw; pa.e1w = e1w; pa.e2w = e2w;
+  pa.txt = txt; pa.w2 = w2; pa.e1b = e1b; pa.ob = ob; pa.tb = tb; pa.inb = inb;
+  pa.W1bf = W1bf; pa.Wqkv = Wqkv; pa.Wo = Wo; pa.Wtxt = Wtxt; pa.Wep1 = Wep1;
+  pa.Wep2 = Wep2; pa.W2t = W2t; pa.Wcomb = Wcomb;
+  pa.ebc = ebc; pa.khv = khv; pa.vhv = vhv;
+  prep<<<1146, 256, 0, stream>>>(pa);
 
   tc1<<<512, 256, 0, stream>>>(fm, W1bf, b1, xP);
 
@@ -795,9 +826,8 @@
     projk<<<1536, 256, 0, stream>>>(gq, gv);
   }
 
-  attn_local<<<512, 256, 0, stream>>>(qk, vhT, oat, oatm);
-
-  globk2<<<8, 256, 0, stream>>>(oatm, khv, vhv, Wo, Wqkv, Wep1, ob, inb, ebc, gcon);
+  attn_lg<<<512, 256, 0, stream>>>(qk, vhT, khv, vhv, Wo, Wqkv, Wep1,
+                                   ob, inb, ebc, oat, oatm, gcon, cnt);
 
   ep12<<<256, 256, 0, stream>>>(oat, Wcomb, Wep2, gcon, e2b, out);
 }
```

Result: slower. 422.9 us (+28.8%).
